# Optimization experiments

Hardware: AMD Instinct MI355X
Metric: run time of the kernel (lower is better)

## Reference

```python
import jax, jax.numpy as jnp
import numpy as np

V = 30522   # bert-base-uncased vocab size
B, S, D, J, K = 2, 512, 768, 12, 4
NUM_LABELS = 7


def setup_inputs() -> dict:
    key = jax.random.key(0)
    ks = jax.random.split(key, 9)
    return {
        "sequence_output": jax.random.normal(ks[0], (B, S, D), jnp.float32),
        "input_ids": jax.random.randint(ks[1], (B, S), 0, V),
        "neighbors": jax.random.randint(ks[2], (B, S, J, K), 0, V),
        "W_mlp": jax.random.normal(ks[3], (J * D, 13 * D), jnp.float32) * 0.02,
        "b_mlp": jnp.zeros((J * D,), jnp.float32),
        "W_attn": jax.random.normal(ks[4], (D, 2 * D), jnp.float32) * 0.02,
        "b_attn": jnp.zeros((D,), jnp.float32),
        "W_cls": jax.random.normal(ks[5], (NUM_LABELS, 2 * D), jnp.float32) * 0.02,
        "b_cls": jnp.zeros((NUM_LABELS,), jnp.float32),
    }


def _gather_neighbors(sequence_output, input_ids, neighbors):
    """Replicates the dict-based gather-sum. The torch dict persists ACROSS
    batch elements (it is never reset), with later positions overwriting
    earlier ones (last occurrence wins). We carry a [V,D] table + presence
    mask through a scan over the batch dim."""
    pos = jnp.arange(S, dtype=jnp.int32)

    def step(carry, xs):
        table, present = carry            # [V,D], [V] bool
        ids, seq, nb = xs                 # [S], [S,D], [S,J,K]
        # last occurrence index of each vocab id in this example (-1 if absent)
        last_idx = jnp.full((V,), -1, jnp.int32).at[ids].max(pos)
        found = last_idx >= 0
        table = jnp.where(found[:, None],
                          seq[jnp.clip(last_idx, 0, S - 1)], table)
        present = present | found
        # sum neighbor embeddings that are present in the dictionary
        emb = jnp.where(present[nb][..., None], table[nb], 0.0).sum(axis=2)  # [S,J,D]
        return (table, present), emb

    init = (jnp.zeros((V, D), sequence_output.dtype), jnp.zeros((V,), bool))
    _, fn = jax.lax.scan(step, init, (input_ids, sequence_output, neighbors))
    return fn                              # [B,S,J,D]


def reference(sequence_output, input_ids, neighbors,
              W_mlp, b_mlp, W_attn, b_attn, W_cls, b_cls):
    fn = _gather_neighbors(sequence_output, input_ids, neighbors)  # [B,S,J,D]
    n_flat = fn.reshape(B, S, J * D)
    # gated MLP: rij = [row ; neighbors], g = sigmoid(W rij), c' = g * n
    rij = jnp.concatenate([sequence_output, n_flat], axis=-1)      # [B,S,13D]
    g = jax.nn.sigmoid(jnp.einsum('bsf,gf->bsg', rij, W_mlp) + b_mlp)
    c = (g * n_flat).reshape(B, S, J, D)                           # [B,S,J,D]
    # Luong-style attention: query = token embedding, context = gated neighbors
    scores = jnp.einsum('bsd,bsjd->bsj', sequence_output, c)
    attn = jax.nn.softmax(scores, axis=-1)
    mix = jnp.einsum('bsj,bsjd->bsd', attn, c)                     # [B,S,D]
    combined = jnp.concatenate([mix, sequence_output], axis=-1)    # [B,S,2D]
    attn_out = jnp.tanh(jnp.einsum('bsf,df->bsd', combined, W_attn) + b_attn)
    final = jnp.concatenate([sequence_output, attn_out], axis=-1)  # [B,S,2D]
    # dropout is identity at inference
    logits = jnp.einsum('bsf,lf->bsl', final, W_cls) + b_cls       # [B,S,7]
    return logits
```

## Files before the change

kernel.cpp:

```cpp
#include <hip/hip_runtime.h>
#include <hip/hip_bf16.h>

#define V_PAD  30528
#define S_LEN  512
#define D_DIM  768
#define J_N    12
#define M_ROWS 1024
#define K_MLP  9984
#define N_MLP  9216
#define K_ATT  1536
#define N_ATT  768
#define N_LBL  7

using bf16x8 = __attribute__((ext_vector_type(8))) __bf16;
using f32x4  = __attribute__((ext_vector_type(4))) float;

__device__ __forceinline__ unsigned short f2bf(float f) {
  union { float f; unsigned int u; } c; c.f = f;
  unsigned int u = c.u;
  return (unsigned short)((u + 0x7fffu + ((u >> 16) & 1u)) >> 16);
}

__global__ __launch_bounds__(256)
void cvt_bf16_kernel(const float* __restrict__ in, unsigned short* __restrict__ out) {
  size_t i = (size_t)blockIdx.x * 256 + threadIdx.x;
  const float4 f0 = ((const float4*)in)[i * 2];
  const float4 f1 = ((const float4*)in)[i * 2 + 1];
  union { unsigned short h[8]; uint4 q; } pk;
  pk.h[0] = f2bf(f0.x); pk.h[1] = f2bf(f0.y); pk.h[2] = f2bf(f0.z); pk.h[3] = f2bf(f0.w);
  pk.h[4] = f2bf(f1.x); pk.h[5] = f2bf(f1.y); pk.h[6] = f2bf(f1.z); pk.h[7] = f2bf(f1.w);
  ((uint4*)out)[i] = pk.q;
}

__global__ void build_tables_kernel(const int* __restrict__ ids,
                                    int* __restrict__ last0,
                                    int* __restrict__ last01) {
  int p = blockIdx.x * 256 + threadIdx.x;
  if (p < M_ROWS) {
    int id = ids[p];
    atomicMax(&last01[id], p);
    if (p < S_LEN) atomicMax(&last0[id], p);
  }
}

__global__ __launch_bounds__(256) void seqrij_kernel(const float* __restrict__ seq,
                                                     unsigned short* __restrict__ rij) {
  int bs = blockIdx.x;
  for (int d = threadIdx.x; d < D_DIM; d += 256)
    rij[(size_t)bs * K_MLP + d] = f2bf(seq[(size_t)bs * D_DIM + d]);
}

__global__ __launch_bounds__(256)
void gather_kernel(const float* __restrict__ seq, const int* __restrict__ nbr,
                   const int* __restrict__ last0, const int* __restrict__ last01,
                   float* __restrict__ nflat, unsigned short* __restrict__ rij) {
  const int bsj = blockIdx.x;
  const int j  = bsj % J_N;
  const int bs = bsj / J_N;
  const int b  = bs >> 9;
  const int* nb = nbr + (size_t)bsj * 4;
  const int* tab = (b == 0) ? last0 : last01;
  const int s0 = tab[nb[0]], s1 = tab[nb[1]], s2 = tab[nb[2]], s3 = tab[nb[3]];
  const int t = threadIdx.x;
#pragma unroll
  for (int u = 0; u < 3; ++u) {
    int d = t + u * 256;
    float acc = 0.f;
    if (s0 >= 0) acc += seq[(size_t)s0 * D_DIM + d];
    if (s1 >= 0) acc += seq[(size_t)s1 * D_DIM + d];
    if (s2 >= 0) acc += seq[(size_t)s2 * D_DIM + d];
    if (s3 >= 0) acc += seq[(size_t)s3 * D_DIM + d];
    nflat[(size_t)bs * N_MLP + j * D_DIM + d] = acc;
    rij[(size_t)bs * K_MLP + D_DIM + j * D_DIM + d] = f2bf(acc);
  }
}

template <int MODE, int TM, int TN, bool BF16B>
__global__ __launch_bounds__(256)
void gemm_nt_kernel(const unsigned short* __restrict__ A,
                    const void* __restrict__ Wv,
                    const float* __restrict__ bias,
                    float* __restrict__ nflat_c,
                    float* __restrict__ outp,
                    int K, int N) {
  constexpr int FM = TM / 32;
  constexpr int FN = TN / 32;
  __shared__ unsigned short ldsA[TM * 32];
  __shared__ unsigned short ldsB[TN * 32];
  const int tid  = threadIdx.x;
  const int lane = tid & 63;
  const int w    = tid >> 6;
  const int m0 = blockIdx.x * TM;
  const int n0 = blockIdx.y * TN;

  f32x4 acc[FM][FN];
#pragma unroll
  for (int i = 0; i < FM; ++i)
#pragma unroll
    for (int j = 0; j < FN; ++j) acc[i][j] = (f32x4){0.f, 0.f, 0.f, 0.f};

  const int lr = lane >> 2;
  const int lc = (lane & 3) * 8;
  const int wm = (w >> 1) * (TM / 2), wn = (w & 1) * (TN / 2);
  const int fr = lane & 15;
  const int fk = (lane >> 4) * 8;

  for (int kk = 0; kk < K; kk += 32) {
#pragma unroll
    for (int q = 0; q < TM / 64; ++q) {
      const int r = w * (TM / 4) + q * 16;
      const unsigned short* g = A + (size_t)(m0 + r + lr) * K + kk + lc;
      __builtin_amdgcn_global_load_lds(
          (const __attribute__((address_space(1))) void*)g,
          (__attribute__((address_space(3))) void*)(&ldsA[r * 32]), 16, 0, 0);
    }
    if (BF16B) {
#pragma unroll
      for (int q = 0; q < TN / 64; ++q) {
        const int r = w * (TN / 4) + q * 16;
        const unsigned short* g = (const unsigned short*)Wv +
                                  (size_t)(n0 + r + lr) * K + kk + lc;
        __builtin_amdgcn_global_load_lds(
            (const __attribute__((address_space(1))) void*)g,
            (__attribute__((address_space(3))) void*)(&ldsB[r * 32]), 16, 0, 0);
      }
    } else {
      constexpr int EPT = TN / 8;
      constexpr int TPR = 32 / EPT;
      const int br = tid / TPR, bc = (tid % TPR) * EPT;
      const float* g = (const float*)Wv + (size_t)(n0 + br) * K + kk + bc;
      union { unsigned short h[EPT]; uint4 q[EPT / 8]; } pk;
#pragma unroll
      for (int e = 0; e < EPT; e += 4) {
        float4 f = *(const float4*)(g + e);
        pk.h[e] = f2bf(f.x); pk.h[e + 1] = f2bf(f.y);
        pk.h[e + 2] = f2bf(f.z); pk.h[e + 3] = f2bf(f.w);
      }
      uint4* dst = (uint4*)&ldsB[br * 32 + bc];
#pragma unroll
      for (int e = 0; e < EPT / 8; ++e) dst[e] = pk.q[e];
    }
    __syncthreads();
    bf16x8 aF[FM], bF[FN];
#pragma unroll
    for (int i = 0; i < FM; ++i) aF[i] = *(const bf16x8*)&ldsA[(wm + i * 16 + fr) * 32 + fk];
#pragma unroll
    for (int j = 0; j < FN; ++j) bF[j] = *(const bf16x8*)&ldsB[(wn + j * 16 + fr) * 32 + fk];
#pragma unroll
    for (int i = 0; i < FM; ++i)
#pragma unroll
      for (int j = 0; j < FN; ++j)
        acc[i][j] = __builtin_amdgcn_mfma_f32_16x16x32_bf16(aF[i], bF[j], acc[i][j], 0, 0, 0);
    __syncthreads();
  }

#pragma unroll
  for (int i = 0; i < FM; ++i) {
    int gm0 = m0 + wm + i * 16 + (lane >> 4) * 4;
#pragma unroll
    for (int j = 0; j < FN; ++j) {
      int gn = n0 + wn + j * 16 + (lane & 15);
      float bv = bias[gn];
#pragma unroll
      for (int r = 0; r < 4; ++r) {
        size_t idx = (size_t)(gm0 + r) * N + gn;
        float x = acc[i][j][r] + bv;
        if (MODE == 0) {
          float gg = 1.0f / (1.0f + __expf(-x));
          nflat_c[idx] = gg * nflat_c[idx];
        } else {
          outp[idx] = tanhf(x);
        }
      }
    }
  }
}

__global__ __launch_bounds__(256)
void attn_kernel(const float* __restrict__ seq, const float* __restrict__ c,
                 unsigned short* __restrict__ combined) {
  __shared__ float sc[N_MLP];
  __shared__ float sq[D_DIM];
  __shared__ float ss[J_N];
  const int m = blockIdx.x;
  const int tid = threadIdx.x, lane = tid & 63, w = tid >> 6;
  const float* crow = c + (size_t)m * N_MLP;
  for (int d = tid; d < N_MLP; d += 256) sc[d] = crow[d];
  for (int d = tid; d < D_DIM; d += 256) sq[d] = seq[(size_t)m * D_DIM + d];
  __syncthreads();
#pragma unroll
  for (int jj = 0; jj < 3; ++jj) {
    int j = w * 3 + jj;
    float p = 0.f;
    for (int d = lane; d < D_DIM; d += 64) p += sq[d] * sc[j * D_DIM + d];
#pragma unroll
    for (int off = 32; off > 0; off >>= 1) p += __shfl_down(p, off);
    if (lane == 0) ss[j] = p;
  }
  __syncthreads();
  float mx = ss[0];
#pragma unroll
  for (int j = 1; j < J_N; ++j) mx = fmaxf(mx, ss[j]);
  float aw[J_N]; float sum = 0.f;
#pragma unroll
  for (int j = 0; j < J_N; ++j) { aw[j] = __expf(ss[j] - mx); sum += aw[j]; }
  float inv = 1.f / sum;
  for (int d = tid; d < D_DIM; d += 256) {
    float mix = 0.f;
#pragma unroll
    for (int j = 0; j < J_N; ++j) mix += aw[j] * sc[j * D_DIM + d];
    combined[(size_t)m * K_ATT + d]         = f2bf(mix * inv);
    combined[(size_t)m * K_ATT + D_DIM + d] = f2bf(sq[d]);
  }
}

__global__ __launch_bounds__(256)
void cls_kernel(const float* __restrict__ seq, const float* __restrict__ attnout,
                const float* __restrict__ Wc, const float* __restrict__ bc,
                float* __restrict__ out) {
  __shared__ float part[N_LBL][256];
  const int m = blockIdx.x, tid = threadIdx.x;
  float p[N_LBL] = {0.f, 0.f, 0.f, 0.f, 0.f, 0.f, 0.f};
  for (int f = tid; f < K_ATT; f += 256) {
    float v = (f < D_DIM) ? seq[(size_t)m * D_DIM + f]
                          : attnout[(size_t)m * D_DIM + (f - D_DIM)];
#pragma unroll
    for (int l = 0; l < N_LBL; ++l) p[l] += v * Wc[l * K_ATT + f];
  }
#pragma unroll
  for (int l = 0; l < N_LBL; ++l) part[l][tid] = p[l];
  __syncthreads();
  for (int s = 128; s > 0; s >>= 1) {
    if (tid < s)
#pragma unroll
      for (int l = 0; l < N_LBL; ++l) part[l][tid] += part[l][tid + s];
    __syncthreads();
  }
  if (tid < N_LBL) out[(size_t)m * N_LBL + tid] = part[tid][0] + bc[tid];
}

extern "C" void kernel_launch(void* const* d_in, const int* in_sizes, int n_in,
                              void* d_out, int out_size, void* d_ws, size_t ws_size,
                              hipStream_t stream) {
  const float* seq   = (const float*)d_in[0];
  const int*   ids   = (const int*)d_in[1];
  const int*   nbr   = (const int*)d_in[2];
  const float* Wmlp  = (const float*)d_in[3];
  const float* bmlp  = (const float*)d_in[4];
  const float* Wattn = (const float*)d_in[5];
  const float* battn = (const float*)d_in[6];
  const float* Wcls  = (const float*)d_in[7];
  const float* bcls  = (const float*)d_in[8];
  float* out = (float*)d_out;

  char* ws = (char*)d_ws;
  size_t off = 0;
  int* last0  = (int*)(ws + off); off += (size_t)V_PAD * 4;
  int* last01 = (int*)(ws + off); off += (size_t)V_PAD * 4;
  unsigned short* rij = (unsigned short*)(ws + off); off += (size_t)M_ROWS * K_MLP * 2;
  float* nflat = (float*)(ws + off); off += (size_t)M_ROWS * N_MLP * 4;
  unsigned short* combined = (unsigned short*)(ws + off); off += (size_t)M_ROWS * K_ATT * 2;
  float* attnout = (float*)(ws + off); off += (size_t)M_ROWS * N_ATT * 4;
  unsigned short* Wb_mlp  = (unsigned short*)(ws + off); off += (size_t)N_MLP * K_MLP * 2;
  unsigned short* Wb_attn = (unsigned short*)(ws + off); off += (size_t)N_ATT * K_ATT * 2;
  const bool big_ws = (ws_size >= off);

  hipMemsetAsync(last0, 0xFF, (size_t)2 * V_PAD * 4, stream);
  build_tables_kernel<<<(M_ROWS + 255) / 256, 256, 0, stream>>>(ids, last0, last01);
  seqrij_kernel<<<M_ROWS, 256, 0, stream>>>(seq, rij);
  gather_kernel<<<M_ROWS * J_N, 256, 0, stream>>>(seq, nbr, last0, last01, nflat, rij);

  if (big_ws) {
    cvt_bf16_kernel<<<(N_MLP * K_MLP) / (256 * 8), 256, 0, stream>>>(Wmlp, Wb_mlp);
    cvt_bf16_kernel<<<(N_ATT * K_ATT) / (256 * 8), 256, 0, stream>>>(Wattn, Wb_attn);
    gemm_nt_kernel<0, 128, 64, true><<<dim3(M_ROWS / 128, N_MLP / 64), 256, 0, stream>>>(
        rij, Wb_mlp, bmlp, nflat, nullptr, K_MLP, N_MLP);
    attn_kernel<<<M_ROWS, 256, 0, stream>>>(seq, nflat, combined);
    gemm_nt_kernel<1, 64, 64, true><<<dim3(M_ROWS / 64, N_ATT / 64), 256, 0, stream>>>(
        combined, Wb_attn, battn, nullptr, attnout, K_ATT, N_ATT);
  } else {
    gemm_nt_kernel<0, 128, 64, false><<<dim3(M_ROWS / 128, N_MLP / 64), 256, 0, stream>>>(
        rij, Wmlp, bmlp, nflat, nullptr, K_MLP, N_MLP);
    attn_kernel<<<M_ROWS, 256, 0, stream>>>(seq, nflat, combined);
    gemm_nt_kernel<1, 64, 64, false><<<dim3(M_ROWS / 64, N_ATT / 64), 256, 0, stream>>>(
        combined, Wattn, battn, nullptr, attnout, K_ATT, N_ATT);
  }
  cls_kernel<<<M_ROWS, 256, 0, stream>>>(seq, attnout, Wcls, bcls, out);
}
```

Before: 970.2 us.

## Split-K MLP GEMM with larger tiles, fuse gating into attention, vectorize gather

```diff
diff --git a/kernel.cpp b/kernel.cpp
--- a/kernel.cpp
+++ b/kernel.cpp
@@ -20,6 +20,9 @@
   unsigned int u = c.u;
   return (unsigned short)((u + 0x7fffu + ((u >> 16) & 1u)) >> 16);
 }
+__device__ __forceinline__ float bf2f(unsigned short h) {
+  union { unsigned int u; float f; } c; c.u = (unsigned int)h << 16; return c.f;
+}
 
 __global__ __launch_bounds__(256)
 void cvt_bf16_kernel(const float* __restrict__ in, unsigned short* __restrict__ out) {
@@ -50,7 +53,8 @@
     rij[(size_t)bs * K_MLP + d] = f2bf(seq[(size_t)bs * D_DIM + d]);
 }
 
-__global__ __launch_bounds__(256)
+template <bool WRITE_NFLAT>
+__global__ __launch_bounds__(192)
 void gather_kernel(const float* __restrict__ seq, const int* __restrict__ nbr,
                    const int* __restrict__ last0, const int* __restrict__ last01,
                    float* __restrict__ nflat, unsigned short* __restrict__ rij) {
@@ -61,18 +65,17 @@
   const int* nb = nbr + (size_t)bsj * 4;
   const int* tab = (b == 0) ? last0 : last01;
   const int s0 = tab[nb[0]], s1 = tab[nb[1]], s2 = tab[nb[2]], s3 = tab[nb[3]];
-  const int t = threadIdx.x;
-#pragma unroll
-  for (int u = 0; u < 3; ++u) {
-    int d = t + u * 256;
-    float acc = 0.f;
-    if (s0 >= 0) acc += seq[(size_t)s0 * D_DIM + d];
-    if (s1 >= 0) acc += seq[(size_t)s1 * D_DIM + d];
-    if (s2 >= 0) acc += seq[(size_t)s2 * D_DIM + d];
-    if (s3 >= 0) acc += seq[(size_t)s3 * D_DIM + d];
-    nflat[(size_t)bs * N_MLP + j * D_DIM + d] = acc;
-    rij[(size_t)bs * K_MLP + D_DIM + j * D_DIM + d] = f2bf(acc);
-  }
+  const int d4 = threadIdx.x;
+  float4 a = {0.f, 0.f, 0.f, 0.f};
+  if (s0 >= 0) { float4 v = ((const float4*)(seq + (size_t)s0 * D_DIM))[d4]; a.x += v.x; a.y += v.y; a.z += v.z; a.w += v.w; }
+  if (s1 >= 0) { float4 v = ((const float4*)(seq + (size_t)s1 * D_DIM))[d4]; a.x += v.x; a.y += v.y; a.z += v.z; a.w += v.w; }
+  if (s2 >= 0) { float4 v = ((const float4*)(seq + (size_t)s2 * D_DIM))[d4]; a.x += v.x; a.y += v.y; a.z += v.z; a.w += v.w; }
+  if (s3 >= 0) { float4 v = ((const float4*)(seq + (size_t)s3 * D_DIM))[d4]; a.x += v.x; a.y += v.y; a.z += v.z; a.w += v.w; }
+  union { unsigned short h[4]; unsigned long long q; } pk;
+  pk.h[0] = f2bf(a.x); pk.h[1] = f2bf(a.y); pk.h[2] = f2bf(a.z); pk.h[3] = f2bf(a.w);
+  *(unsigned long long*)(rij + (size_t)bs * K_MLP + D_DIM + j * D_DIM + d4 * 4) = pk.q;
+  if (WRITE_NFLAT)
+    ((float4*)(nflat + (size_t)bs * N_MLP + j * D_DIM))[d4] = a;
 }
 
 template <int MODE, int TM, int TN, bool BF16B>
@@ -82,7 +85,7 @@
                     const float* __restrict__ bias,
                     float* __restrict__ nflat_c,
                     float* __restrict__ outp,
-                    int K, int N) {
+                    int K, int N, int kchunk) {
   constexpr int FM = TM / 32;
   constexpr int FN = TN / 32;
   __shared__ unsigned short ldsA[TM * 32];
@@ -92,6 +95,7 @@
   const int w    = tid >> 6;
   const int m0 = blockIdx.x * TM;
   const int n0 = blockIdx.y * TN;
+  const int kb = blockIdx.z * kchunk;
 
   f32x4 acc[FM][FN];
 #pragma unroll
@@ -105,7 +109,7 @@
   const int fr = lane & 15;
   const int fk = (lane >> 4) * 8;
 
-  for (int kk = 0; kk < K; kk += 32) {
+  for (int kk = kb; kk < kb + kchunk; kk += 32) {
 #pragma unroll
     for (int q = 0; q < TM / 64; ++q) {
       const int r = w * (TM / 4) + q * 16;
@@ -154,13 +158,14 @@
     __syncthreads();
   }
 
+  const size_t zoff = (MODE == 2) ? (size_t)blockIdx.z * M_ROWS * N : 0;
 #pragma unroll
   for (int i = 0; i < FM; ++i) {
     int gm0 = m0 + wm + i * 16 + (lane >> 4) * 4;
 #pragma unroll
     for (int j = 0; j < FN; ++j) {
       int gn = n0 + wn + j * 16 + (lane & 15);
-      float bv = bias[gn];
+      float bv = (MODE == 2) ? 0.f : bias[gn];
 #pragma unroll
       for (int r = 0; r < 4; ++r) {
         size_t idx = (size_t)(gm0 + r) * N + gn;
@@ -168,11 +173,60 @@
         if (MODE == 0) {
           float gg = 1.0f / (1.0f + __expf(-x));
           nflat_c[idx] = gg * nflat_c[idx];
+        } else if (MODE == 1) {
+          outp[idx] = tanhf(x);
         } else {
-          outp[idx] = tanhf(x);
+          outp[zoff + idx] = x;
         }
       }
     }
+  }
+}
+
+__global__ __launch_bounds__(256)
+void attn_fused_kernel(const float* __restrict__ seq,
+                       const float* __restrict__ p0, const float* __restrict__ p1,
+                       const float* __restrict__ bmlp,
+                       const unsigned short* __restrict__ rij,
+                       unsigned short* __restrict__ combined) {
+  __shared__ float sc[N_MLP];
+  __shared__ float sq[D_DIM];
+  __shared__ float ss[J_N];
+  const int m = blockIdx.x;
+  const int tid = threadIdx.x, lane = tid & 63, w = tid >> 6;
+  for (int d = tid; d < D_DIM; d += 256) sq[d] = seq[(size_t)m * D_DIM + d];
+  const float* q0 = p0 + (size_t)m * N_MLP;
+  const float* q1 = p1 + (size_t)m * N_MLP;
+  const unsigned short* nrow = rij + (size_t)m * K_MLP + D_DIM;
+  for (int d = tid; d < N_MLP; d += 256) {
+    float z = q0[d] + q1[d] + bmlp[d];
+    float g = 1.0f / (1.0f + __expf(-z));
+    sc[d] = g * bf2f(nrow[d]);
+  }
+  __syncthreads();
+#pragma unroll
+  for (int jj = 0; jj < 3; ++jj) {
+    int j = w * 3 + jj;
+    float p = 0.f;
+    for (int d = lane; d < D_DIM; d += 64) p += sq[d] * sc[j * D_DIM + d];
+#pragma unroll
+    for (int off = 32; off > 0; off >>= 1) p += __shfl_down(p, off);
+    if (lane == 0) ss[j] = p;
+  }
+  __syncthreads();
+  float mx = ss[0];
+#pragma unroll
+  for (int j = 1; j < J_N; ++j) mx = fmaxf(mx, ss[j]);
+  float aw[J_N]; float sum = 0.f;
+#pragma unroll
+  for (int j = 0; j < J_N; ++j) { aw[j] = __expf(ss[j] - mx); sum += aw[j]; }
+  float inv = 1.f / sum;
+  for (int d = tid; d < D_DIM; d += 256) {
+    float mix = 0.f;
+#pragma unroll
+    for (int j = 0; j < J_N; ++j) mix += aw[j] * sc[j * D_DIM + d];
+    combined[(size_t)m * K_ATT + d]         = f2bf(mix * inv);
+    combined[(size_t)m * K_ATT + D_DIM + d] = f2bf(sq[d]);
   }
 }
 
@@ -218,8 +272,8 @@
 void cls_kernel(const float* __restrict__ seq, const float* __restrict__ attnout,
                 const float* __restrict__ Wc, const float* __restrict__ bc,
                 float* __restrict__ out) {
-  __shared__ float part[N_LBL][256];
-  const int m = blockIdx.x, tid = threadIdx.x;
+  __shared__ float part[4][N_LBL];
+  const int m = blockIdx.x, tid = threadIdx.x, lane = tid & 63, w = tid >> 6;
   float p[N_LBL] = {0.f, 0.f, 0.f, 0.f, 0.f, 0.f, 0.f};
   for (int f = tid; f < K_ATT; f += 256) {
     float v = (f < D_DIM) ? seq[(size_t)m * D_DIM + f]
@@ -228,15 +282,18 @@
     for (int l = 0; l < N_LBL; ++l) p[l] += v * Wc[l * K_ATT + f];
   }
 #pragma unroll
-  for (int l = 0; l < N_LBL; ++l) part[l][tid] = p[l];
-  __syncthreads();
-  for (int s = 128; s > 0; s >>= 1) {
-    if (tid < s)
-#pragma unroll
-      for (int l = 0; l < N_LBL; ++l) part[l][tid] += part[l][tid + s];
-    __syncthreads();
-  }
-  if (tid < N_LBL) out[(size_t)m * N_LBL + tid] = part[tid][0] + bc[tid];
+  for (int l = 0; l < N_LBL; ++l) {
+#pragma unroll
+    for (int off = 32; off > 0; off >>= 1) p[l] += __shfl_down(p[l], off);
+  }
+  if (lane == 0) {
+#pragma unroll
+    for (int l = 0; l < N_LBL; ++l) part[w][l] = p[l];
+  }
+  __syncthreads();
+  if (tid < N_LBL)
+    out[(size_t)m * N_LBL + tid] =
+        part[0][tid] + part[1][tid] + part[2][tid] + part[3][tid] + bc[tid];
 }
 
 extern "C" void kernel_launch(void* const* d_in, const int* in_sizes, int n_in,
@@ -258,32 +315,52 @@
   int* last0  = (int*)(ws + off); off += (size_t)V_PAD * 4;
   int* last01 = (int*)(ws + off); off += (size_t)V_PAD * 4;
   unsigned short* rij = (unsigned short*)(ws + off); off += (size_t)M_ROWS * K_MLP * 2;
-  float* nflat = (float*)(ws + off); off += (size_t)M_ROWS * N_MLP * 4;
   unsigned short* combined = (unsigned short*)(ws + off); off += (size_t)M_ROWS * K_ATT * 2;
   float* attnout = (float*)(ws + off); off += (size_t)M_ROWS * N_ATT * 4;
-  unsigned short* Wb_mlp  = (unsigned short*)(ws + off); off += (size_t)N_MLP * K_MLP * 2;
-  unsigned short* Wb_attn = (unsigned short*)(ws + off); off += (size_t)N_ATT * K_ATT * 2;
-  const bool big_ws = (ws_size >= off);
+  const size_t common = off;
+
+  size_t ob = common;
+  unsigned short* Wb_mlp  = (unsigned short*)(ws + ob); ob += (size_t)N_MLP * K_MLP * 2;
+  unsigned short* Wb_attn = (unsigned short*)(ws + ob); ob += (size_t)N_ATT * K_ATT * 2;
+  float* p0 = (float*)(ws + ob); ob += (size_t)M_ROWS * N_MLP * 4;
+  float* p1 = (float*)(ws + ob); ob += (size_t)M_ROWS * N_MLP * 4;
+  size_t om = common;
+  float* nflat_m = (float*)(ws + om); om += (size_t)M_ROWS * N_MLP * 4;
+  unsigned short* Wm_mlp  = (unsigned short*)(ws + om); om += (size_t)N_MLP * K_MLP * 2;
+  unsigned short* Wm_attn = (unsigned short*)(ws + om); om += (size_t)N_ATT * K_ATT * 2;
+  size_t os = common + (size_t)M_ROWS * N_MLP * 4;
 
   hipMemsetAsync(last0, 0xFF, (size_t)2 * V_PAD * 4, stream);
   build_tables_kernel<<<(M_ROWS + 255) / 256, 256, 0, stream>>>(ids, last0, last01);
   seqrij_kernel<<<M_ROWS, 256, 0, stream>>>(seq, rij);
-  gather_kernel<<<M_ROWS * J_N, 256, 0, stream>>>(seq, nbr, last0, last01, nflat, rij);
-
-  if (big_ws) {
+
+  if (ws_size >= ob) {
+    gather_kernel<false><<<M_ROWS * J_N, 192, 0, stream>>>(seq, nbr, last0, last01, nullptr, rij);
     cvt_bf16_kernel<<<(N_MLP * K_MLP) / (256 * 8), 256, 0, stream>>>(Wmlp, Wb_mlp);
     cvt_bf16_kernel<<<(N_ATT * K_ATT) / (256 * 8), 256, 0, stream>>>(Wattn, Wb_attn);
+    gemm_nt_kernel<2, 128, 128, true><<<dim3(M_ROWS / 128, N_MLP / 128, 2), 256, 0, stream>>>(
+        rij, Wb_mlp, nullptr, nullptr, p0, K_MLP, N_MLP, K_MLP / 2);
+    attn_fused_kernel<<<M_ROWS, 256, 0, stream>>>(seq, p0, p1, bmlp, rij, combined);
+    gemm_nt_kernel<1, 64, 64, true><<<dim3(M_ROWS / 64, N_ATT / 64), 256, 0, stream>>>(
+        combined, Wb_attn, battn, nullptr, attnout, K_ATT, N_ATT, K_ATT);
+  } else if (ws_size >= om) {
+    gather_kernel<true><<<M_ROWS * J_N, 192, 0, stream>>>(seq, nbr, last0, last01, nflat_m, rij);
+    cvt_bf16_kernel<<<(N_MLP * K_MLP) / (256 * 8), 256, 0, stream>>>(Wmlp, Wm_mlp);
+    cvt_bf16_kernel<<<(N_ATT * K_ATT) / (256 * 8), 256, 0, stream>>>(Wattn, Wm_attn);
     gemm_nt_kernel<0, 128, 64, true><<<dim3(M_ROWS / 128, N_MLP / 64), 256, 0, stream>>>(
-        rij, Wb_mlp, bmlp, nflat, nullptr, K_MLP, N_MLP);
-    attn_kernel<<<M_ROWS, 256, 0, stream>>>(seq, nflat, combined);
+        rij, Wm_mlp, bmlp, nflat_m, nullptr, K_MLP, N_MLP, K_MLP);
+    attn_kernel<<<M_ROWS, 256, 0, stream>>>(seq, nflat_m, combined);
     gemm_nt_kernel<1, 64, 64, true><<<dim3(M_ROWS / 64, N_ATT / 64), 256, 0, stream>>>(
-        combined, Wb_attn, battn, nullptr, attnout, K_ATT, N_ATT);
+        combined, Wm_attn, battn, nullptr, attnout, K_ATT, N_ATT, K_ATT);
   } else {
+    float* nflat_s = nflat_m;
+    (void)os;
+    gather_kernel<true><<<M_ROWS * J_N, 192, 0, stream>>>(seq, nbr, last0, last01, nflat_s, rij);
     gemm_nt_kernel<0, 128, 64, false><<<dim3(M_ROWS / 128, N_MLP / 64), 256, 0, stream>>>(
-        rij, Wmlp, bmlp, nflat, nullptr, K_MLP, N_MLP);
-    attn_kernel<<<M_ROWS, 256, 0, stream>>>(seq, nflat, combined);
+        rij, Wmlp, bmlp, nflat_s, nullptr, K_MLP, N_MLP, K_MLP);
+    attn_kernel<<<M_ROWS, 256, 0, stream>>>(seq, nflat_s, combined);
     gemm_nt_kernel<1, 64, 64, false><<<dim3(M_ROWS / 64, N_ATT / 64), 256, 0, stream>>>(
-        combined, Wattn, battn, nullptr, attnout, K_ATT, N_ATT);
+        combined, Wattn, battn, nullptr, attnout, K_ATT, N_ATT, K_ATT);
   }
   cls_kernel<<<M_ROWS, 256, 0, stream>>>(seq, attnout, Wcls, bcls, out);
 }
```

After: 901.1 us. 7.1% less time.
